# Performance work log

Measured on AMD Instinct MI355X. Metric: run time of the kernel, lower is better.

The kernel has to match this reference:

```python
import jax, jax.numpy as jnp
import numpy as np

N_NODES = 100000


def sage_conv(x, edge_index, Wl, bl, Wr):
    # PyG SAGEConv (aggr='mean', root_weight=True):
    #   out_i = lin_l(mean_{j in N(i)} x_j) + lin_r(x_i)
    src, dst = edge_index[0], edge_index[1]
    msgs = x[src]  # [E, C] gather of source-node features
    summed = jax.ops.segment_sum(msgs, dst, num_segments=N_NODES)
    deg = jax.ops.segment_sum(jnp.ones((edge_index.shape[1],), x.dtype), dst,
                              num_segments=N_NODES)
    mean = summed / jnp.maximum(deg, 1.0)[:, None]  # zero rows stay zero
    return mean @ Wl.T + bl + x @ Wr.T


def setup_inputs() -> dict:
    key = jax.random.key(0)
    ks = jax.random.split(key, 12)
    IN, HID, OUT = 128, 128, 64
    E, P = 1600000, 200000
    x = jax.random.normal(ks[0], (N_NODES, IN), jnp.float32)
    edge_index = jax.random.randint(ks[1], (2, E), 0, N_NODES)
    edge_label_index = jax.random.randint(ks[2], (2, P), 0, N_NODES)
    s1 = 1.0 / np.sqrt(IN)
    s2 = 1.0 / np.sqrt(HID)
    s3 = 1.0 / np.sqrt(2 * OUT)
    return {
        "x": x,
        "edge_index": edge_index,
        "edge_label_index": edge_label_index,
        "Wl1": jax.random.uniform(ks[3], (HID, IN), jnp.float32, -s1, s1),
        "bl1": jnp.zeros((HID,), jnp.float32),
        "Wr1": jax.random.uniform(ks[4], (HID, IN), jnp.float32, -s1, s1),
        "Wl2": jax.random.uniform(ks[5], (OUT, HID), jnp.float32, -s2, s2),
        "bl2": jnp.zeros((OUT,), jnp.float32),
        "Wr2": jax.random.uniform(ks[6], (OUT, HID), jnp.float32, -s2, s2),
        "Wdec": jax.random.uniform(ks[7], (1, 2 * OUT), jnp.float32, -s3, s3),
        "bdec": jax.random.uniform(ks[8], (1,), jnp.float32, -s3, s3),
    }


def reference(x, edge_index, edge_label_index, Wl1, bl1, Wr1, Wl2, bl2, Wr2,
              Wdec, bdec):
    # encode: SAGEConv -> relu -> (dropout p=0) -> SAGEConv
    h = jax.nn.relu(sage_conv(x, edge_index, Wl1, bl1, Wr1))
    z = sage_conv(h, edge_index, Wl2, bl2, Wr2)
    # decode: gather endpoint embeddings, concat, linear -> [P]
    feats = jnp.concatenate([z[edge_label_index[0]], z[edge_label_index[1]]],
                            axis=-1)
    return (feats @ Wdec.T + bdec).reshape(-1)
```

## Files before the change

kernel.cpp:

```cpp
#include <hip/hip_runtime.h>

#define NN 100000
#define NBUK ((NN + 255) / 256)
#define BCAP 5120

typedef unsigned short u16;
typedef unsigned int u32;
typedef __attribute__((ext_vector_type(8))) short short8v;
typedef __attribute__((ext_vector_type(4))) float float4v;

__device__ __forceinline__ u32 f2bf_rne(float f) {
    u32 x = __float_as_uint(f);
    return (x + 0x7fffu + ((x >> 16) & 1u)) >> 16;
}
__device__ __forceinline__ float bf2f(u32 u) {
    return __uint_as_float(u << 16);
}
__device__ __forceinline__ uint4 pack8u(const float4& a, const float4& b) {
    uint4 u;
    u.x = f2bf_rne(a.x) | (f2bf_rne(a.y) << 16);
    u.y = f2bf_rne(a.z) | (f2bf_rne(a.w) << 16);
    u.z = f2bf_rne(b.x) | (f2bf_rne(b.y) << 16);
    u.w = f2bf_rne(b.z) | (f2bf_rne(b.w) << 16);
    return u;
}

__global__ void zero_buckets_kernel(int* __restrict__ p) {
    int i = threadIdx.x;
    if (i < NBUK) p[i] = 0;
}

__global__ __launch_bounds__(256) void partition_kernel(const int* __restrict__ edges,
                                                        int* __restrict__ bucketCnt,
                                                        int* __restrict__ bucketed, int E) {
    __shared__ int h[NBUK];
    __shared__ int base[NBUK];
    for (int i = threadIdx.x; i < NBUK; i += 256) h[i] = 0;
    __syncthreads();
    int b0 = blockIdx.x * 4096;
    for (int k = threadIdx.x; k < 4096; k += 256) {
        int e = b0 + k;
        if (e < E) atomicAdd(&h[edges[E + e] >> 8], 1);
    }
    __syncthreads();
    for (int i = threadIdx.x; i < NBUK; i += 256) {
        int c = h[i];
        base[i] = c ? (i * BCAP + atomicAdd(&bucketCnt[i], c)) : 0;
        h[i] = 0;
    }
    __syncthreads();
    for (int k = threadIdx.x; k < 4096; k += 256) {
        int e = b0 + k;
        if (e < E) {
            int d = edges[E + e];
            int b = d >> 8;
            int off = atomicAdd(&h[b], 1);
            bucketed[base[b] + off] = edges[e] | ((d & 255) << 20);
        }
    }
}

__global__ __launch_bounds__(256) void bucket_sort_kernel(const int* __restrict__ bucketed,
                                                          const int* __restrict__ bucketCnt,
                                                          int* __restrict__ rowStart,
                                                          int* __restrict__ cnt,
                                                          int* __restrict__ sortedSrc, int N) {
    __shared__ int h[256];
    __shared__ int pos[256];
    int b = blockIdx.x;
    int tid = threadIdx.x;
    int start = b * BCAP, end = start + bucketCnt[b];
    h[tid] = 0;
    __syncthreads();
    for (int k = start + tid; k < end; k += 256) atomicAdd(&h[bucketed[k] >> 20], 1);
    __syncthreads();
    int v = h[tid];
    pos[tid] = v;
    __syncthreads();
    for (int off = 1; off < 256; off <<= 1) {
        int t = (tid >= off) ? pos[tid - off] : 0;
        __syncthreads();
        pos[tid] += t;
        __syncthreads();
    }
    int excl = start + pos[tid] - v;
    int node = (b << 8) + tid;
    if (node < N) {
        rowStart[node] = excl;
        cnt[node] = v;
    }
    h[tid] = excl;
    __syncthreads();
    for (int k = start + tid; k < end; k += 256) {
        int entry = bucketed[k];
        int p = atomicAdd(&h[entry >> 20], 1);
        sortedSrc[p] = entry & 0xFFFFF;
    }
}

template <bool XF32>
__global__ __launch_bounds__(256, 2) void gemm_mfma_kernel(
    const void* __restrict__ Xv, const float* __restrict__ Wa,
    const float* __restrict__ Wb, int CHALF,
    u16* __restrict__ Ob, int OSTRIDE, int N)
{
    __shared__ u16 As[128 * 128];

    const int tid = threadIdx.x;
    const int w = tid >> 6;
    const int l = tid & 63;
    const int l15 = l & 15;
    const int lhi = l >> 4;
    const int rowBase = blockIdx.x * 128;
    const int cBase = blockIdx.y * 128;
    char* asb = reinterpret_cast<char*>(As);

#pragma unroll
    for (int i = 0; i < 8; ++i) {
        int q = tid + i * 256;
        int r = q >> 4, c = q & 15;
        int gr = rowBase + r;
        uint4 pk = make_uint4(0u, 0u, 0u, 0u);
        if (gr < N) {
            if (XF32) {
                const float* xf = (const float*)Xv + (size_t)gr * 128 + c * 8;
                float4 f0 = *reinterpret_cast<const float4*>(xf);
                float4 f1 = *reinterpret_cast<const float4*>(xf + 4);
                pk = pack8u(f0, f1);
            } else {
                pk = *reinterpret_cast<const uint4*>((const u16*)Xv + (size_t)gr * 128 + c * 8);
            }
        }
        *reinterpret_cast<uint4*>(asb + r * 256 + ((c * 16) ^ ((r & 7) << 4))) = pk;
    }

    short8v bfrag[2][4];
#pragma unroll
    for (int nj = 0; nj < 2; ++nj) {
        int c = cBase + w * 32 + nj * 16 + l15;
        const float* wr = (c < CHALF) ? (Wa + (size_t)c * 128)
                                      : (Wb + (size_t)(c - CHALF) * 128);
#pragma unroll
        for (int kk = 0; kk < 4; ++kk) {
            float4 f0 = *reinterpret_cast<const float4*>(wr + kk * 32 + lhi * 8);
            float4 f1 = *reinterpret_cast<const float4*>(wr + kk * 32 + lhi * 8 + 4);
            uint4 pk = pack8u(f0, f1);
            union { uint4 u; short8v s; } cv; cv.u = pk;
            bfrag[nj][kk] = cv.s;
        }
    }

    __syncthreads();

    float4v acc[8][2];
    const float4v az = {0.f, 0.f, 0.f, 0.f};
#pragma unroll
    for (int mi = 0; mi < 8; ++mi) { acc[mi][0] = az; acc[mi][1] = az; }

#pragma unroll
    for (int kk = 0; kk < 4; ++kk) {
#pragma unroll
        for (int mi = 0; mi < 8; ++mi) {
            int r = mi * 16 + l15;
            short8v a = *reinterpret_cast<const short8v*>(
                asb + r * 256 + ((kk * 64 + lhi * 16) ^ ((r & 7) << 4)));
            acc[mi][0] = __builtin_amdgcn_mfma_f32_16x16x32_bf16(a, bfrag[0][kk], acc[mi][0], 0, 0, 0);
            acc[mi][1] = __builtin_amdgcn_mfma_f32_16x16x32_bf16(a, bfrag[1][kk], acc[mi][1], 0, 0, 0);
        }
    }

#pragma unroll
    for (int mi = 0; mi < 8; ++mi) {
#pragma unroll
        for (int nj = 0; nj < 2; ++nj) {
            int gc = cBase + w * 32 + nj * 16 + l15;
#pragma unroll
            for (int j = 0; j < 4; ++j) {
                int gr = rowBase + mi * 16 + lhi * 4 + j;
                if (gr < N) Ob[(size_t)gr * OSTRIDE + gc] = (u16)f2bf_rne(acc[mi][nj][j]);
            }
        }
    }
}

template <int C, bool RELU, bool OUTBF>
__global__ __launch_bounds__(256) void agg_combine_kernel(
    const u16* __restrict__ T, int tStride,
    const u16* __restrict__ R,
    const int* __restrict__ sortedSrc, const int* __restrict__ rowStart,
    const int* __restrict__ cnt, const float* __restrict__ bias,
    float* __restrict__ outF, u16* __restrict__ outB, int N)
{
    constexpr int TPN = C / 8;
    constexpr int NPB = 256 / TPN;
    int n = blockIdx.x * NPB + threadIdx.x / TPN;
    int c = threadIdx.x % TPN;
    if (n >= N) return;
    int start = rowStart[n];
    int m = cnt[n];
    const int* __restrict__ ep = sortedSrc + start;
    const u16* __restrict__ tp = T + c * 8;

    float a0 = 0.f, a1 = 0.f, a2 = 0.f, a3 = 0.f;
    float a4 = 0.f, a5 = 0.f, a6 = 0.f, a7 = 0.f;
    int k = 0;
    for (; k + 4 <= m; k += 4) {
        int s0 = ep[k], s1 = ep[k + 1], s2 = ep[k + 2], s3 = ep[k + 3];
        uint4 v0 = *reinterpret_cast<const uint4*>(&tp[(size_t)s0 * tStride]);
        uint4 v1 = *reinterpret_cast<const uint4*>(&tp[(size_t)s1 * tStride]);
        uint4 v2 = *reinterpret_cast<const uint4*>(&tp[(size_t)s2 * tStride]);
        uint4 v3 = *reinterpret_cast<const uint4*>(&tp[(size_t)s3 * tStride]);
        a0 += bf2f(v0.x & 0xffffu) + bf2f(v1.x & 0xffffu) + bf2f(v2.x & 0xffffu) + bf2f(v3.x & 0xffffu);
        a1 += bf2f(v0.x >> 16) + bf2f(v1.x >> 16) + bf2f(v2.x >> 16) + bf2f(v3.x >> 16);
        a2 += bf2f(v0.y & 0xffffu) + bf2f(v1.y & 0xffffu) + bf2f(v2.y & 0xffffu) + bf2f(v3.y & 0xffffu);
        a3 += bf2f(v0.y >> 16) + bf2f(v1.y >> 16) + bf2f(v2.y >> 16) + bf2f(v3.y >> 16);
        a4 += bf2f(v0.z & 0xffffu) + bf2f(v1.z & 0xffffu) + bf2f(v2.z & 0xffffu) + bf2f(v3.z & 0xffffu);
        a5 += bf2f(v0.z >> 16) + bf2f(v1.z >> 16) + bf2f(v2.z >> 16) + bf2f(v3.z >> 16);
        a6 += bf2f(v0.w & 0xffffu) + bf2f(v1.w & 0xffffu) + bf2f(v2.w & 0xffffu) + bf2f(v3.w & 0xffffu);
        a7 += bf2f(v0.w >> 16) + bf2f(v1.w >> 16) + bf2f(v2.w >> 16) + bf2f(v3.w >> 16);
    }
    for (; k < m; ++k) {
        uint4 v = *reinterpret_cast<const uint4*>(&tp[(size_t)ep[k] * tStride]);
        a0 += bf2f(v.x & 0xffffu); a1 += bf2f(v.x >> 16);
        a2 += bf2f(v.y & 0xffffu); a3 += bf2f(v.y >> 16);
        a4 += bf2f(v.z & 0xffffu); a5 += bf2f(v.z >> 16);
        a6 += bf2f(v.w & 0xffffu); a7 += bf2f(v.w >> 16);
    }
    float inv = 1.0f / fmaxf((float)m, 1.0f);
    uint4 rv = *reinterpret_cast<const uint4*>(&R[(size_t)n * tStride + c * 8]);
    float o0 = fmaf(a0, inv, bias[c * 8 + 0]) + bf2f(rv.x & 0xffffu);
    float o1 = fmaf(a1, inv, bias[c * 8 + 1]) + bf2f(rv.x >> 16);
    float o2 = fmaf(a2, inv, bias[c * 8 + 2]) + bf2f(rv.y & 0xffffu);
    float o3 = fmaf(a3, inv, bias[c * 8 + 3]) + bf2f(rv.y >> 16);
    float o4 = fmaf(a4, inv, bias[c * 8 + 4]) + bf2f(rv.z & 0xffffu);
    float o5 = fmaf(a5, inv, bias[c * 8 + 5]) + bf2f(rv.z >> 16);
    float o6 = fmaf(a6, inv, bias[c * 8 + 6]) + bf2f(rv.w & 0xffffu);
    float o7 = fmaf(a7, inv, bias[c * 8 + 7]) + bf2f(rv.w >> 16);
    if (RELU) {
        o0 = fmaxf(o0, 0.f); o1 = fmaxf(o1, 0.f);
        o2 = fmaxf(o2, 0.f); o3 = fmaxf(o3, 0.f);
        o4 = fmaxf(o4, 0.f); o5 = fmaxf(o5, 0.f);
        o6 = fmaxf(o6, 0.f); o7 = fmaxf(o7, 0.f);
    }
    if (OUTBF) {
        uint4 o;
        o.x = f2bf_rne(o0) | (f2bf_rne(o1) << 16);
        o.y = f2bf_rne(o2) | (f2bf_rne(o3) << 16);
        o.z = f2bf_rne(o4) | (f2bf_rne(o5) << 16);
        o.w = f2bf_rne(o6) | (f2bf_rne(o7) << 16);
        *reinterpret_cast<uint4*>(&outB[(size_t)n * C + c * 8]) = o;
    } else {
        float4 lo = make_float4(o0, o1, o2, o3);
        float4 hi = make_float4(o4, o5, o6, o7);
        float* p = &outF[(size_t)n * C + c * 8];
        *reinterpret_cast<float4*>(p) = lo;
        *reinterpret_cast<float4*>(p + 4) = hi;
    }
}

__global__ __launch_bounds__(256) void decode_kernel(
    const u16* __restrict__ z, const int* __restrict__ eli,
    const float* __restrict__ Wdec, const float* __restrict__ bdec,
    float* __restrict__ out, int P)
{
    int t = blockIdx.x * 256 + threadIdx.x;
    int p = t >> 6;
    int lane = t & 63;
    if (p >= P) return;
    int a = eli[p];
    int b = eli[P + p];
    float acc = bf2f(z[(size_t)a * 64 + lane]) * Wdec[lane]
              + bf2f(z[(size_t)b * 64 + lane]) * Wdec[64 + lane];
    for (int off = 32; off; off >>= 1) acc += __shfl_down(acc, off);
    if (lane == 0) out[p] = acc + bdec[0];
}

extern "C" void kernel_launch(void* const* d_in, const int* in_sizes, int n_in,
                              void* d_out, int out_size, void* d_ws, size_t ws_size,
                              hipStream_t stream) {
    const float* x    = (const float*)d_in[0];
    const int*   ei   = (const int*)d_in[1];
    const int*   eli  = (const int*)d_in[2];
    const float* Wl1  = (const float*)d_in[3];
    const float* bl1  = (const float*)d_in[4];
    const float* Wr1  = (const float*)d_in[5];
    const float* Wl2  = (const float*)d_in[6];
    const float* bl2  = (const float*)d_in[7];
    const float* Wr2  = (const float*)d_in[8];
    const float* Wdec = (const float*)d_in[9];
    const float* bdec = (const float*)d_in[10];
    float* out = (float*)d_out;

    const int N = NN;
    const int E = in_sizes[1] / 2;
    const int P = in_sizes[2] / 2;
    const int EB = (E + 4095) / 4096;

    char* wp = (char*)d_ws;
    u16* obf = (u16*)wp;  wp += (size_t)N * 256 * 2;
    u16* hbf = (u16*)wp;  wp += (size_t)N * 128 * 2;
    u16* zb  = (u16*)wp;  wp += (size_t)N * 64 * 2;
    int* bucketCnt = (int*)wp;
    int* rowStart  = bucketCnt + NBUK;
    int* cnt       = rowStart + N;
    int* bucketed  = cnt + N;
    int* sortedSrc = bucketed + NBUK * BCAP;

    zero_buckets_kernel<<<1, 512, 0, stream>>>(bucketCnt);
    partition_kernel<<<EB, 256, 0, stream>>>(ei, bucketCnt, bucketed, E);
    bucket_sort_kernel<<<NBUK, 256, 0, stream>>>(bucketed, bucketCnt, rowStart, cnt, sortedSrc, N);

    {
        dim3 grid((N + 127) / 128, 2);
        gemm_mfma_kernel<true><<<grid, 256, 0, stream>>>(x, Wl1, Wr1, 128, obf, 256, N);
    }
    agg_combine_kernel<128, true, true><<<(N + 15) / 16, 256, 0, stream>>>(
        obf, 256, obf + 128, sortedSrc, rowStart, cnt, bl1, nullptr, hbf, N);

    {
        dim3 grid((N + 127) / 128, 1);
        gemm_mfma_kernel<false><<<grid, 256, 0, stream>>>(hbf, Wl2, Wr2, 64, obf, 128, N);
    }
    agg_combine_kernel<64, false, true><<<(N + 31) / 32, 256, 0, stream>>>(
        obf, 128, obf + 64, sortedSrc, rowStart, cnt, bl2, nullptr, zb, N);

    decode_kernel<<<(P + 3) / 4, 256, 0, stream>>>(zb, eli, Wdec, bdec, out, P);
}
```

Measured before the change: 236.0 us.

## Split layer-1 aggregation into two 64-column passes and unroll gathers by eight

The layer-1 aggregate-combine now runs as two launches, each covering 64 of the 128 feature columns. This halves the per-pass gathered working set, so it should fit better in the cache. The gather loop also gains an 8-way unrolled main body that issues eight independent row loads before accumulating, to raise memory-level parallelism. The cost is that edge indices and counts are read twice for layer 1, plus one extra kernel launch, and the unroll uses more registers.

```diff
diff --git a/kernel.cpp b/kernel.cpp
--- a/kernel.cpp
+++ b/kernel.cpp
@@ -183,15 +183,15 @@
     }
 }
 
-template <int C, bool RELU, bool OUTBF>
+template <bool RELU>
 __global__ __launch_bounds__(256) void agg_combine_kernel(
     const u16* __restrict__ T, int tStride,
     const u16* __restrict__ R,
     const int* __restrict__ sortedSrc, const int* __restrict__ rowStart,
     const int* __restrict__ cnt, const float* __restrict__ bias,
-    float* __restrict__ outF, u16* __restrict__ outB, int N)
+    u16* __restrict__ outB, int oStride, int N)
 {
-    constexpr int TPN = C / 8;
+    constexpr int TPN = 8;
     constexpr int NPB = 256 / TPN;
     int n = blockIdx.x * NPB + threadIdx.x / TPN;
     int c = threadIdx.x % TPN;
@@ -204,20 +204,42 @@
     float a0 = 0.f, a1 = 0.f, a2 = 0.f, a3 = 0.f;
     float a4 = 0.f, a5 = 0.f, a6 = 0.f, a7 = 0.f;
     int k = 0;
+    for (; k + 8 <= m; k += 8) {
+        int s[8];
+        uint4 v[8];
+#pragma unroll
+        for (int u = 0; u < 8; ++u) s[u] = ep[k + u];
+#pragma unroll
+        for (int u = 0; u < 8; ++u)
+            v[u] = *reinterpret_cast<const uint4*>(&tp[(size_t)s[u] * tStride]);
+#pragma unroll
+        for (int h = 0; h < 2; ++h) {
+            const uint4& w0 = v[h * 4 + 0]; const uint4& w1 = v[h * 4 + 1];
+            const uint4& w2 = v[h * 4 + 2]; const uint4& w3 = v[h * 4 + 3];
+            a0 += bf2f(w0.x & 0xffffu) + bf2f(w1.x & 0xffffu) + bf2f(w2.x & 0xffffu) + bf2f(w3.x & 0xffffu);
+            a1 += bf2f(w0.x >> 16) + bf2f(w1.x >> 16) + bf2f(w2.x >> 16) + bf2f(w3.x >> 16);
+            a2 += bf2f(w0.y & 0xffffu) + bf2f(w1.y & 0xffffu) + bf2f(w2.y & 0xffffu) + bf2f(w3.y & 0xffffu);
+            a3 += bf2f(w0.y >> 16) + bf2f(w1.y >> 16) + bf2f(w2.y >> 16) + bf2f(w3.y >> 16);
+            a4 += bf2f(w0.z & 0xffffu) + bf2f(w1.z & 0xffffu) + bf2f(w2.z & 0xffffu) + bf2f(w3.z & 0xffffu);
+            a5 += bf2f(w0.z >> 16) + bf2f(w1.z >> 16) + bf2f(w2.z >> 16) + bf2f(w3.z >> 16);
+            a6 += bf2f(w0.w & 0xffffu) + bf2f(w1.w & 0xffffu) + bf2f(w2.w & 0xffffu) + bf2f(w3.w & 0xffffu);
+            a7 += bf2f(w0.w >> 16) + bf2f(w1.w >> 16) + bf2f(w2.w >> 16) + bf2f(w3.w >> 16);
+        }
+    }
     for (; k + 4 <= m; k += 4) {
         int s0 = ep[k], s1 = ep[k + 1], s2 = ep[k + 2], s3 = ep[k + 3];
-        uint4 v0 = *reinterpret_cast<const uint4*>(&tp[(size_t)s0 * tStride]);
-        uint4 v1 = *reinterpret_cast<const uint4*>(&tp[(size_t)s1 * tStride]);
-        uint4 v2 = *reinterpret_cast<const uint4*>(&tp[(size_t)s2 * tStride]);
-        uint4 v3 = *reinterpret_cast<const uint4*>(&tp[(size_t)s3 * tStride]);
-        a0 += bf2f(v0.x & 0xffffu) + bf2f(v1.x & 0xffffu) + bf2f(v2.x & 0xffffu) + bf2f(v3.x & 0xffffu);
-        a1 += bf2f(v0.x >> 16) + bf2f(v1.x >> 16) + bf2f(v2.x >> 16) + bf2f(v3.x >> 16);
-        a2 += bf2f(v0.y & 0xffffu) + bf2f(v1.y & 0xffffu) + bf2f(v2.y & 0xffffu) + bf2f(v3.y & 0xffffu);
-        a3 += bf2f(v0.y >> 16) + bf2f(v1.y >> 16) + bf2f(v2.y >> 16) + bf2f(v3.y >> 16);
-        a4 += bf2f(v0.z & 0xffffu) + bf2f(v1.z & 0xffffu) + bf2f(v2.z & 0xffffu) + bf2f(v3.z & 0xffffu);
-        a5 += bf2f(v0.z >> 16) + bf2f(v1.z >> 16) + bf2f(v2.z >> 16) + bf2f(v3.z >> 16);
-        a6 += bf2f(v0.w & 0xffffu) + bf2f(v1.w & 0xffffu) + bf2f(v2.w & 0xffffu) + bf2f(v3.w & 0xffffu);
-        a7 += bf2f(v0.w >> 16) + bf2f(v1.w >> 16) + bf2f(v2.w >> 16) + bf2f(v3.w >> 16);
+        uint4 w0 = *reinterpret_cast<const uint4*>(&tp[(size_t)s0 * tStride]);
+        uint4 w1 = *reinterpret_cast<const uint4*>(&tp[(size_t)s1 * tStride]);
+        uint4 w2 = *reinterpret_cast<const uint4*>(&tp[(size_t)s2 * tStride]);
+        uint4 w3 = *reinterpret_cast<const uint4*>(&tp[(size_t)s3 * tStride]);
+        a0 += bf2f(w0.x & 0xffffu) + bf2f(w1.x & 0xffffu) + bf2f(w2.x & 0xffffu) + bf2f(w3.x & 0xffffu);
+        a1 += bf2f(w0.x >> 16) + bf2f(w1.x >> 16) + bf2f(w2.x >> 16) + bf2f(w3.x >> 16);
+        a2 += bf2f(w0.y & 0xffffu) + bf2f(w1.y & 0xffffu) + bf2f(w2.y & 0xffffu) + bf2f(w3.y & 0xffffu);
+        a3 += bf2f(w0.y >> 16) + bf2f(w1.y >> 16) + bf2f(w2.y >> 16) + bf2f(w3.y >> 16);
+        a4 += bf2f(w0.z & 0xffffu) + bf2f(w1.z & 0xffffu) + bf2f(w2.z & 0xffffu) + bf2f(w3.z & 0xffffu);
+        a5 += bf2f(w0.z >> 16) + bf2f(w1.z >> 16) + bf2f(w2.z >> 16) + bf2f(w3.z >> 16);
+        a6 += bf2f(w0.w & 0xffffu) + bf2f(w1.w & 0xffffu) + bf2f(w2.w & 0xffffu) + bf2f(w3.w & 0xffffu);
+        a7 += bf2f(w0.w >> 16) + bf2f(w1.w >> 16) + bf2f(w2.w >> 16) + bf2f(w3.w >> 16);
     }
     for (; k < m; ++k) {
         uint4 v = *reinterpret_cast<const uint4*>(&tp[(size_t)ep[k] * tStride]);
@@ -242,20 +264,12 @@
         o4 = fmaxf(o4, 0.f); o5 = fmaxf(o5, 0.f);
         o6 = fmaxf(o6, 0.f); o7 = fmaxf(o7, 0.f);
     }
-    if (OUTBF) {
-        uint4 o;
-        o.x = f2bf_rne(o0) | (f2bf_rne(o1) << 16);
-        o.y = f2bf_rne(o2) | (f2bf_rne(o3) << 16);
-        o.z = f2bf_rne(o4) | (f2bf_rne(o5) << 16);
-        o.w = f2bf_rne(o6) | (f2bf_rne(o7) << 16);
-        *reinterpret_cast<uint4*>(&outB[(size_t)n * C + c * 8]) = o;
-    } else {
-        float4 lo = make_float4(o0, o1, o2, o3);
-        float4 hi = make_float4(o4, o5, o6, o7);
-        float* p = &outF[(size_t)n * C + c * 8];
-        *reinterpret_cast<float4*>(p) = lo;
-        *reinterpret_cast<float4*>(p + 4) = hi;
-    }
+    uint4 o;
+    o.x = f2bf_rne(o0) | (f2bf_rne(o1) << 16);
+    o.y = f2bf_rne(o2) | (f2bf_rne(o3) << 16);
+    o.z = f2bf_rne(o4) | (f2bf_rne(o5) << 16);
+    o.w = f2bf_rne(o6) | (f2bf_rne(o7) << 16);
+    *reinterpret_cast<uint4*>(&outB[(size_t)n * oStride + c * 8]) = o;
 }
 
 __global__ __launch_bounds__(256) void decode_kernel(
@@ -314,15 +328,17 @@
         dim3 grid((N + 127) / 128, 2);
         gemm_mfma_kernel<true><<<grid, 256, 0, stream>>>(x, Wl1, Wr1, 128, obf, 256, N);
     }
-    agg_combine_kernel<128, true, true><<<(N + 15) / 16, 256, 0, stream>>>(
-        obf, 256, obf + 128, sortedSrc, rowStart, cnt, bl1, nullptr, hbf, N);
+    agg_combine_kernel<true><<<(N + 31) / 32, 256, 0, stream>>>(
+        obf, 256, obf + 128, sortedSrc, rowStart, cnt, bl1, hbf, 128, N);
+    agg_combine_kernel<true><<<(N + 31) / 32, 256, 0, stream>>>(
+        obf + 64, 256, obf + 192, sortedSrc, rowStart, cnt, bl1 + 64, hbf + 64, 128, N);
 
     {
         dim3 grid((N + 127) / 128, 1);
         gemm_mfma_kernel<false><<<grid, 256, 0, stream>>>(hbf, Wl2, Wr2, 64, obf, 128, N);
     }
-    agg_combine_kernel<64, false, true><<<(N + 31) / 32, 256, 0, stream>>>(
-        obf, 128, obf + 64, sortedSrc, rowStart, cnt, bl2, nullptr, zb, N);
+    agg_combine_kernel<false><<<(N + 31) / 32, 256, 0, stream>>>(
+        obf, 128, obf + 64, sortedSrc, rowStart, cnt, bl2, zb, 64, N);
 
     decode_kernel<<<(P + 3) / 4, 256, 0, stream>>>(zb, eli, Wdec, bdec, out, P);
 }
```

Result: slower. 241.9 us (+2.5%).
